# Optimization experiments

Measured on AMD Instinct MI355X. Metric: run time of the kernel, lower is better.

## Reference

```python
import jax, jax.numpy as jnp
import numpy as np

B, S, D, H, L, FF = 1, 2048, 512, 8, 4, 2048
DH = D // H


def _sincos(n, d):
    theta = 1.0 / (10000.0 ** (np.arange(0, d, 2, dtype=np.float64) / d))
    ang = np.arange(n, dtype=np.float64)[:, None] * theta[None, :]
    sin = np.repeat(np.sin(ang), 2, axis=-1).astype(np.float32)
    cos = np.repeat(np.cos(ang), 2, axis=-1).astype(np.float32)
    return jnp.asarray(sin), jnp.asarray(cos)  # [n, d]


def _rot(x):
    # rotate pairs: (x1, x2) -> (-x2, x1), interleaved
    x1, x2 = x[..., 0::2], x[..., 1::2]
    return jnp.stack([-x2, x1], axis=-1).reshape(x.shape)


def _theta_shift(x, sin, cos):
    return x * cos + _rot(x) * sin


def _decay_mask(n, h):
    # RetNet per-head decay gammas: 1 - exp(linspace(log(1/32), log(1/512), h))
    gammas = 1.0 - np.exp(np.linspace(np.log(1.0 / 32.0), np.log(1.0 / 512.0), h))
    dist = np.arange(n)[:, None] - np.arange(n)[None, :]
    m = np.where(dist >= 0, gammas[:, None, None] ** np.maximum(dist, 0), 0.0)
    return jnp.asarray(m, dtype=jnp.float32)  # [h, n, n]


def _ln(x, w, b, eps=1e-5):
    mu = x.mean(-1, keepdims=True)
    var = ((x - mu) ** 2).mean(-1, keepdims=True)
    return (x - mu) * jax.lax.rsqrt(var + eps) * w + b


def setup_inputs() -> dict:
    key = jax.random.key(0)
    ks = jax.random.split(key, 12)
    sc = 0.02
    nrm = lambda k, shp: jax.random.normal(k, shp, jnp.float32) * sc
    return {
        "x": jax.random.normal(ks[0], (B, S, D), jnp.float32),
        "pos_emb": nrm(ks[1], (5000, D)),
        "Wq": nrm(ks[2], (L, D, D)), "bq": jnp.zeros((L, D), jnp.float32),
        "Wk": nrm(ks[3], (L, D, D)), "bk": jnp.zeros((L, D), jnp.float32),
        "Wv": nrm(ks[4], (L, D, D)), "bv": jnp.zeros((L, D), jnp.float32),
        "Wg": nrm(ks[5], (L, D, D)), "bg": jnp.zeros((L, D), jnp.float32),
        "Wo": nrm(ks[6], (L, D, D)), "bo": jnp.zeros((L, D), jnp.float32),
        "ln1w": jnp.ones((L, D), jnp.float32), "ln1b": jnp.zeros((L, D), jnp.float32),
        "ln2w": jnp.ones((L, D), jnp.float32), "ln2b": jnp.zeros((L, D), jnp.float32),
        "W1": nrm(ks[7], (L, D, FF)), "b1": jnp.zeros((L, FF), jnp.float32),
        "W2": nrm(ks[8], (L, FF, D)), "b2": jnp.zeros((L, D), jnp.float32),
        "Wout": nrm(ks[9], (D, 1)), "bout": jnp.zeros((1,), jnp.float32),
    }


def reference(x, pos_emb, Wq, bq, Wk, bk, Wv, bv, Wg, bg, Wo, bo,
              ln1w, ln1b, ln2w, ln2b, W1, b1, W2, b2, Wout, bout):
    b, s, d = x.shape
    # faithful to source: pos_emb[:x.shape[0]] (requires B==1 to broadcast)
    x = x + pos_emb[: x.shape[0]]
    sin, cos = _sincos(s, DH)
    dmask = _decay_mask(s, H)  # [h, s, s]
    inv_scale = 1.0 / jnp.sqrt(jnp.float32(DH))

    def heads(t):  # [b,s,d] -> [b,h,s,dh]
        return t.reshape(b, s, H, DH).transpose(0, 2, 1, 3)

    for l in range(L):
        # --- multi-scale retention block (pre-LN) ---
        y = _ln(x, ln1w[l], ln1b[l])
        q = heads(y @ Wq[l] + bq[l])
        k = heads(y @ Wk[l] + bk[l])
        v = heads(y @ Wv[l] + bv[l])
        q = _theta_shift(q, sin, cos) * inv_scale
        k = _theta_shift(k, sin, cos)
        sim = jnp.einsum("bhnd,bhmd->bhnm", q, k) * dmask  # decay-masked QK^T
        ret = jnp.einsum("bhnm,bhmd->bhnd", sim, v)
        # per-head group norm (no affine)
        mu = ret.mean(-1, keepdims=True)
        var = ((ret - mu) ** 2).mean(-1, keepdims=True)
        ret = (ret - mu) * jax.lax.rsqrt(var + 1e-6)
        ret = ret.transpose(0, 2, 1, 3).reshape(b, s, d)
        g = jax.nn.silu(y @ Wg[l] + bg[l])
        x = x + (g * ret) @ Wo[l] + bo[l]
        # --- FFN block (pre-LN, swish) ---
        z = _ln(x, ln2w[l], ln2b[l])
        x = x + jax.nn.silu(z @ W1[l] + b1[l]) @ W2[l] + b2[l]

    return jax.nn.sigmoid(x @ Wout + bout)  # [b, s, 1]
```

## Files before the change

kernel.cpp:

```cpp
#include <hip/hip_runtime.h>
#include <math.h>
#include <stdint.h>

#define SEQ 2048
#define DMODEL 512
#define NH 8
#define DHEAD 64
#define NL 4
#define DFF 2048

typedef __attribute__((ext_vector_type(8))) short short8;
typedef __attribute__((ext_vector_type(4))) float f32x4;

__device__ __forceinline__ short f2bf(float f) {
  unsigned u = __float_as_uint(f);
  u += 0x7fffu + ((u >> 16) & 1u);
  return (short)(u >> 16);
}
__device__ __forceinline__ float silu_f(float x) { return x / (1.f + __expf(-x)); }

__device__ __forceinline__ void cp16(const void* g, void* l) {
  __builtin_amdgcn_global_load_lds(
      (const __attribute__((address_space(1))) unsigned*)(unsigned long long)(uintptr_t)g,
      (__attribute__((address_space(3))) unsigned*)(unsigned)(uintptr_t)l, 16, 0, 0);
}

struct TP { const float* src; short* dst; int rows, cols, base, lstride; };
struct TPs { TP t[7]; };
__global__ __launch_bounds__(256) void k_prep(TPs ts, float* __restrict__ sn, float* __restrict__ cs) {
  int bid = blockIdx.x;
  if (bid >= 13312) {
    int g = (bid - 13312) * 256 + threadIdx.x;
    int s = g >> 5, p = g & 31;
    double inv = pow(10000.0, -(double)p / 32.0);
    double a = (double)s * inv;
    float sv = (float)sin(a), cv = (float)cos(a);
    sn[s * DHEAD + 2 * p] = sv; sn[s * DHEAD + 2 * p + 1] = sv;
    cs[s * DHEAD + 2 * p] = cv; cs[s * DHEAD + 2 * p + 1] = cv;
    return;
  }
  int di = 6;
  while (di > 0 && bid < ts.t[di].base) --di;
  TP d = ts.t[di];
  int local = bid - d.base;
  int tx = d.cols >> 5, ty = d.rows >> 5;
  int tpz = tx * ty;
  int z = local / tpz, rem = local - z * tpz;
  int bx = (rem % tx) * 32, by = (rem / tx) * 32;
  const float* src = d.src + (size_t)z * d.rows * d.cols;
  short* dst = d.dst + (size_t)z * d.lstride;
  __shared__ float tile[32][33];
  int txi = threadIdx.x & 31, tyi = threadIdx.x >> 5;
#pragma unroll
  for (int k = 0; k < 4; ++k)
    tile[tyi + k * 8][txi] = src[(size_t)(by + tyi + k * 8) * d.cols + bx + txi];
  __syncthreads();
#pragma unroll
  for (int k = 0; k < 4; ++k)
    dst[(size_t)(bx + tyi + k * 8) * d.rows + by + txi] = f2bf(tile[txi][tyi + k * 8]);
}

__global__ __launch_bounds__(256) void k_ln(const float* __restrict__ x, const float* __restrict__ parts, int np,
                                            const float* __restrict__ w, const float* __restrict__ b,
                                            short* __restrict__ o, float eps, float* __restrict__ xout,
                                            const float* __restrict__ pos) {
  int wid = threadIdx.x >> 6, lane = threadIdx.x & 63;
  int row = blockIdx.x * 4 + wid;
  size_t base = (size_t)row * DMODEL + lane * 8;
  float4 v0 = *(const float4*)(x + base);
  float4 v1 = *(const float4*)(x + base + 4);
  if (pos) {
    float4 p0 = *(const float4*)(pos + lane * 8);
    float4 p1 = *(const float4*)(pos + lane * 8 + 4);
    v0.x += p0.x; v0.y += p0.y; v0.z += p0.z; v0.w += p0.w;
    v1.x += p1.x; v1.y += p1.y; v1.z += p1.z; v1.w += p1.w;
  }
  for (int p = 0; p < np; ++p) {
    const float* pp = parts + (size_t)p * SEQ * DMODEL;
    float4 a0 = *(const float4*)(pp + base);
    float4 a1 = *(const float4*)(pp + base + 4);
    v0.x += a0.x; v0.y += a0.y; v0.z += a0.z; v0.w += a0.w;
    v1.x += a1.x; v1.y += a1.y; v1.z += a1.z; v1.w += a1.w;
  }
  if (xout) {
    *(float4*)(xout + base) = v0;
    *(float4*)(xout + base + 4) = v1;
  }
  float sm = v0.x + v0.y + v0.z + v0.w + v1.x + v1.y + v1.z + v1.w;
  float sq = v0.x * v0.x + v0.y * v0.y + v0.z * v0.z + v0.w * v0.w +
             v1.x * v1.x + v1.y * v1.y + v1.z * v1.z + v1.w * v1.w;
#pragma unroll
  for (int m = 1; m < 64; m <<= 1) { sm += __shfl_xor(sm, m); sq += __shfl_xor(sq, m); }
  float mu = sm * (1.f / 512.f);
  float rstd = rsqrtf(sq * (1.f / 512.f) - mu * mu + eps);
  const float* wr = w + lane * 8; const float* br = b + lane * 8;
  float vals[8] = {v0.x, v0.y, v0.z, v0.w, v1.x, v1.y, v1.z, v1.w};
  short t[8] __attribute__((aligned(16)));
#pragma unroll
  for (int i = 0; i < 8; ++i) t[i] = f2bf((vals[i] - mu) * rstd * wr[i] + br[i]);
  *(int4*)(o + (size_t)row * DMODEL + lane * 8) = *(int4*)t;
}

struct GB { const short* Bt; const float* bias; void* out; int mode; };
struct GP {
  const short* A;
  const float* sn; const float* cs;
  GB b[4];
  int M, N, K, kspl, wide;
};

template <int BN>
__global__ __launch_bounds__(256) void k_gemm(GP ga) {
  constexpr int NBW = BN / 32;
  constexpr int BRND = BN / 32;
  const int z = blockIdx.z;
  const int n0 = blockIdx.x * BN, m0 = blockIdx.y * 64;
  GB gb; int k0, klen;
  if (ga.kspl > 0) { gb = ga.b[0]; k0 = z * ga.kspl; klen = ga.kspl; }
  else { gb = ga.wide ? ga.b[n0 >> 9] : ga.b[z]; k0 = 0; klen = ga.K; }
  const int K = ga.K, N = ga.N, M = ga.M;
  const int tid = threadIdx.x;
  const int w = tid >> 6, lane = tid & 63, l16 = lane & 15, quad = lane >> 4;
  const int wm = (w & 1) * 32, wn = (w >> 1) * (BN / 2);
  const int nIter = klen >> 6;

  __shared__ __align__(16) short As[2][4096];
  __shared__ __align__(16) short Bs[2][BN * 64];

  const short* Ab = ga.A + (size_t)m0 * K + k0;
  const short* Bb = gb.Bt + (size_t)n0 * K + k0;
  const int rsub = lane >> 3, cch = (lane & 7) ^ rsub;

  auto stage = [&](int buf, int it) {
#pragma unroll
    for (int c = 0; c < 2; ++c) {
      int seg = w + 4 * c;
      cp16(Ab + (size_t)(seg * 8 + rsub) * K + (it << 6) + cch * 8, &As[buf][seg * 512]);
    }
#pragma unroll
    for (int c = 0; c < BRND; ++c) {
      int seg = w + 4 * c;
      cp16(Bb + (size_t)(seg * 8 + rsub) * K + (it << 6) + cch * 8, &Bs[buf][seg * 512]);
    }
  };

  f32x4 acc[2][NBW];
#pragma unroll
  for (int a = 0; a < 2; ++a)
#pragma unroll
    for (int b = 0; b < NBW; ++b) acc[a][b] = {0.f, 0.f, 0.f, 0.f};

  stage(0, 0);
  for (int it = 0; it < nIter; ++it) {
    __syncthreads();
    if (it + 1 < nIter) stage((it + 1) & 1, it + 1);
    const short* as = As[it & 1];
    const short* bs = Bs[it & 1];
#pragma unroll
    for (int kki = 0; kki < 2; ++kki) {
      int ch = ((quad + 4 * kki) ^ (l16 & 7)) * 8;
      short8 af[2], bfv[NBW];
#pragma unroll
      for (int a = 0; a < 2; ++a) af[a] = *(const short8*)&as[(wm + a * 16 + l16) * 64 + ch];
#pragma unroll
      for (int b = 0; b < NBW; ++b) bfv[b] = *(const short8*)&bs[(wn + b * 16 + l16) * 64 + ch];
#pragma unroll
      for (int a = 0; a < 2; ++a)
#pragma unroll
        for (int b = 0; b < NBW; ++b)
          acc[a][b] = __builtin_amdgcn_mfma_f32_16x16x32_bf16(af[a], bfv[b], acc[a][b], 0, 0, 0);
    }
  }

  const int mode = gb.mode;
#pragma unroll
  for (int a = 0; a < 2; ++a) {
#pragma unroll
    for (int b = 0; b < NBW; ++b) {
      int row0 = m0 + wm + a * 16 + quad * 4;
      int col = n0 + wn + b * 16 + l16;
      int colO = ga.wide ? (col & 511) : col;
      float bi = (mode == 2 && z > 0) ? 0.f : gb.bias[colO];
      float vals[4];
#pragma unroll
      for (int r = 0; r < 4; ++r) vals[r] = acc[a][b][r] + bi;
      if (mode == 5 || mode == 6) {
        float sc = (mode == 5) ? 0.125f : 1.f;
        int d = colO & 63;
#pragma unroll
        for (int r = 0; r < 4; ++r) {
          int s = row0 + r;
          float vv = vals[r];
          float p = __shfl_xor(vv, 1);
          float rot = (colO & 1) ? p : -p;
          float o = (vv * ga.cs[s * 64 + d] + rot * ga.sn[s * 64 + d]) * sc;
          ((short*)gb.out)[(size_t)s * DMODEL + colO] = f2bf(o);
        }
      } else if (mode == 4) {
        short t4[4] __attribute__((aligned(8)));
#pragma unroll
        for (int r = 0; r < 4; ++r) t4[r] = f2bf(vals[r]);
        *(uint2*)&((short*)gb.out)[(size_t)colO * M + row0] = *(const uint2*)t4;
      } else if (mode == 0) {
#pragma unroll
        for (int r = 0; r < 4; ++r) ((float*)gb.out)[(size_t)(row0 + r) * DMODEL + colO] = vals[r];
      } else if (mode == 1) {
#pragma unroll
        for (int r = 0; r < 4; ++r) ((short*)gb.out)[(size_t)(row0 + r) * N + col] = f2bf(silu_f(vals[r]));
      } else {
        float* po = (float*)gb.out + (size_t)z * M * DMODEL;
#pragma unroll
        for (int r = 0; r < 4; ++r) po[(size_t)(row0 + r) * DMODEL + colO] = vals[r];
      }
    }
  }
}

__global__ __launch_bounds__(256) void k_attn(const short* __restrict__ qb, const short* __restrict__ kb,
                                              const short* __restrict__ vtb, float* __restrict__ r0,
                                              float* __restrict__ r1) {
  int x = blockIdx.x, hd = blockIdx.y, jc = blockIdx.z;
  int ib = jc ? (31 - x) : x;
  int t = threadIdx.x;
  int w = t >> 6, lane = t & 63, l16 = lane & 15, quad = lane >> 4;
  __shared__ __align__(16) short smem[4 * 64 * 72];
  short* qs = smem;
  short* kt = smem + 4608;
  short* vt = smem + 9216;
  short* p  = smem + 13824;

  double stepd = (log(1.0 / 512.0) - log(1.0 / 32.0)) / 7.0;
  double gam = 1.0 - exp(log(1.0 / 32.0) + hd * stepd);
  float l2g = (float)(log(gam) * 1.4426950408889634);

  for (int c = t; c < 512; c += 256) {
    int r = c >> 3, d8 = (c & 7) * 8;
    *(short8*)&qs[r * 72 + d8] = *(const short8*)&qb[(size_t)(ib * 64 + r) * DMODEL + hd * DHEAD + d8];
  }
  f32x4 oacc[4];
#pragma unroll
  for (int b = 0; b < 4; ++b) oacc[b] = {0.f, 0.f, 0.f, 0.f};

  for (int jb = jc; jb <= ib; jb += 2) {
    __syncthreads();
    for (int c = t; c < 512; c += 256) {
      int r = c >> 3, d8 = (c & 7) * 8;
      *(short8*)&kt[r * 72 + d8] = *(const short8*)&kb[(size_t)(jb * 64 + r) * DMODEL + hd * DHEAD + d8];
      *(short8*)&vt[r * 72 + d8] = *(const short8*)&vtb[(size_t)(hd * DHEAD + r) * SEQ + jb * 64 + d8];
    }
    __syncthreads();
    f32x4 sacc[4];
#pragma unroll
    for (int b = 0; b < 4; ++b) sacc[b] = {0.f, 0.f, 0.f, 0.f};
#pragma unroll
    for (int kk = 0; kk < 64; kk += 32) {
      short8 af = *(const short8*)&qs[(w * 16 + l16) * 72 + kk + quad * 8];
#pragma unroll
      for (int b = 0; b < 4; ++b) {
        short8 bf_ = *(const short8*)&kt[(b * 16 + l16) * 72 + kk + quad * 8];
        sacc[b] = __builtin_amdgcn_mfma_f32_16x16x32_bf16(af, bf_, sacc[b], 0, 0, 0);
      }
    }
    int dtile = (ib - jb) * 64;
#pragma unroll
    for (int b = 0; b < 4; ++b) {
#pragma unroll
      for (int r = 0; r < 4; ++r) {
        int iloc = w * 16 + quad * 4 + r;
        int jloc = b * 16 + l16;
        int df = dtile + iloc - jloc;
        float dec = (df < 0) ? 0.f : exp2f(l2g * (float)df);
        p[iloc * 72 + jloc] = f2bf(sacc[b][r] * dec);
      }
    }
    __syncthreads();
#pragma unroll
    for (int kk = 0; kk < 64; kk += 32) {
      short8 af = *(const short8*)&vt[(w * 16 + l16) * 72 + kk + quad * 8];
#pragma unroll
      for (int b = 0; b < 4; ++b) {
        short8 bf_ = *(const short8*)&p[(b * 16 + l16) * 72 + kk + quad * 8];
        oacc[b] = __builtin_amdgcn_mfma_f32_16x16x32_bf16(af, bf_, oacc[b], 0, 0, 0);
      }
    }
  }
  __syncthreads();
  float* obuf = (float*)smem;
#pragma unroll
  for (int b = 0; b < 4; ++b) {
#pragma unroll
    for (int r = 0; r < 4; ++r) {
      int d = w * 16 + quad * 4 + r;
      int i = b * 16 + l16;
      obuf[i * 68 + d] = oacc[b][r];
    }
  }
  __syncthreads();
  float* rp = jc ? r1 : r0;
  for (int c = t; c < 1024; c += 256) {
    int r = c >> 4, d4 = (c & 15) * 4;
    *(float4*)&rp[(size_t)(ib * 64 + r) * DMODEL + hd * DHEAD + d4] = *(const float4*)&obuf[r * 68 + d4];
  }
}

__global__ __launch_bounds__(256) void k_retgate(const float* __restrict__ r0, const float* __restrict__ r1,
                                                 const float* __restrict__ g, short* __restrict__ o) {
  int wid = threadIdx.x >> 6, lane = threadIdx.x & 63;
  int row = blockIdx.x * 4 + wid;
  int s = row >> 3, hd = row & 7;
  size_t base = (size_t)s * DMODEL + hd * DHEAD + lane;
  float v = r0[base] + r1[base];
  float sm = v, sq = v * v;
#pragma unroll
  for (int m = 1; m < 64; m <<= 1) { sm += __shfl_xor(sm, m); sq += __shfl_xor(sq, m); }
  float mu = sm * (1.f / 64.f);
  float var = sq * (1.f / 64.f) - mu * mu;
  float rn = (v - mu) * rsqrtf(var + 1e-6f);
  o[base] = f2bf(silu_f(g[base]) * rn);
}

__global__ __launch_bounds__(256) void k_final(const float* __restrict__ x, const float* __restrict__ parts, int np,
                                               const float* __restrict__ w, const float* __restrict__ bo,
                                               float* __restrict__ o) {
  int wid = threadIdx.x >> 6, lane = threadIdx.x & 63;
  int row = blockIdx.x * 4 + wid;
  size_t base = (size_t)row * DMODEL + lane * 8;
  float4 a0 = *(const float4*)(x + base), a1 = *(const float4*)(x + base + 4);
  for (int p = 0; p < np; ++p) {
    const float* pp = parts + (size_t)p * SEQ * DMODEL;
    float4 b0 = *(const float4*)(pp + base);
    float4 b1 = *(const float4*)(pp + base + 4);
    a0.x += b0.x; a0.y += b0.y; a0.z += b0.z; a0.w += b0.w;
    a1.x += b1.x; a1.y += b1.y; a1.z += b1.z; a1.w += b1.w;
  }
  float4 w0 = *(const float4*)(w + lane * 8), w1 = *(const float4*)(w + lane * 8 + 4);
  float sm = a0.x * w0.x + a0.y * w0.y + a0.z * w0.z + a0.w * w0.w +
             a1.x * w1.x + a1.y * w1.y + a1.z * w1.z + a1.w * w1.w;
#pragma unroll
  for (int m = 1; m < 64; m <<= 1) sm += __shfl_xor(sm, m);
  if (lane == 0) o[row] = 1.f / (1.f + __expf(-(sm + bo[0])));
}

extern "C" void kernel_launch(void* const* d_in, const int* in_sizes, int n_in,
                              void* d_out, int out_size, void* d_ws, size_t ws_size,
                              hipStream_t stream) {
  const float* x_in = (const float*)d_in[0];
  const float* pos = (const float*)d_in[1];
  const float* Wq = (const float*)d_in[2];  const float* bq = (const float*)d_in[3];
  const float* Wk = (const float*)d_in[4];  const float* bk = (const float*)d_in[5];
  const float* Wv = (const float*)d_in[6];  const float* bv = (const float*)d_in[7];
  const float* Wg = (const float*)d_in[8];  const float* bg = (const float*)d_in[9];
  const float* Wo = (const float*)d_in[10]; const float* bo = (const float*)d_in[11];
  const float* ln1w = (const float*)d_in[12]; const float* ln1b = (const float*)d_in[13];
  const float* ln2w = (const float*)d_in[14]; const float* ln2b = (const float*)d_in[15];
  const float* W1 = (const float*)d_in[16]; const float* b1 = (const float*)d_in[17];
  const float* W2 = (const float*)d_in[18]; const float* b2 = (const float*)d_in[19];
  const float* Wout = (const float*)d_in[20]; const float* bout = (const float*)d_in[21];
  float* out = (float*)d_out;

  char* ws = (char*)d_ws;
  size_t off = 0;
  auto alloc = [&](size_t bytes) -> void* {
    void* p = ws + off;
    off += (bytes + 255) & ~(size_t)255;
    return p;
  };
  const size_t DD = (size_t)DMODEL * DMODEL;
  const size_t SD = (size_t)SEQ * DMODEL;
  short* wqkvg = (short*)alloc((size_t)NL * 4 * DD * 2);
  short* wot = (short*)alloc((size_t)NL * DD * 2);
  short* w1t = (short*)alloc((size_t)NL * DMODEL * DFF * 2);
  short* w2t = (short*)alloc((size_t)NL * DMODEL * DFF * 2);
  float* xb = (float*)alloc(SD * 4);
  short* ybf = (short*)alloc(SD * 2);
  float* graw = (float*)alloc(SD * 4);
  short* qb = (short*)alloc(SD * 2);
  short* kb = (short*)alloc(SD * 2);
  short* vtb = (short*)alloc(SD * 2);
  float* ret0 = (float*)alloc(SD * 4);
  float* ret1 = (float*)alloc(SD * 4);
  short* grb = (short*)alloc(SD * 2);
  short* zbf = (short*)alloc(SD * 2);
  short* hbf = (short*)alloc((size_t)SEQ * DFF * 2);
  float* sint = (float*)alloc((size_t)SEQ * DHEAD * 4);
  float* cost = (float*)alloc((size_t)SEQ * DHEAD * 4);
  float* wpart = (float*)alloc(2 * SD * 4);
  float* fpart = (float*)alloc(4 * SD * 4);

  TPs tp;
  tp.t[0] = TP{Wq, wqkvg + 0 * DD, DMODEL, DMODEL, 0, (int)(4 * DD)};
  tp.t[1] = TP{Wk, wqkvg + 1 * DD, DMODEL, DMODEL, 1024, (int)(4 * DD)};
  tp.t[2] = TP{Wv, wqkvg + 2 * DD, DMODEL, DMODEL, 2048, (int)(4 * DD)};
  tp.t[3] = TP{Wg, wqkvg + 3 * DD, DMODEL, DMODEL, 3072, (int)(4 * DD)};
  tp.t[4] = TP{Wo, wot, DMODEL, DMODEL, 4096, (int)DD};
  tp.t[5] = TP{W1, w1t, DMODEL, DFF, 5120, DMODEL * DFF};
  tp.t[6] = TP{W2, w2t, DFF, DMODEL, 9216, DMODEL * DFF};
  k_prep<<<13568, 256, 0, stream>>>(tp, sint, cost);

  for (int l = 0; l < NL; ++l) {
    k_ln<<<SEQ / 4, 256, 0, stream>>>(l == 0 ? x_in : xb, fpart, l == 0 ? 0 : 4,
                                      ln1w + l * DMODEL, ln1b + l * DMODEL, ybf, 1e-5f,
                                      xb, l == 0 ? pos : nullptr);

    GP gq{};
    gq.A = ybf; gq.sn = sint; gq.cs = cost;
    gq.b[0] = GB{wqkvg + (size_t)l * 4 * DD, bq + l * DMODEL, qb, 5};
    gq.b[1] = GB{wqkvg + (size_t)l * 4 * DD, bk + l * DMODEL, kb, 6};
    gq.b[2] = GB{wqkvg + (size_t)l * 4 * DD, bv + l * DMODEL, vtb, 4};
    gq.b[3] = GB{wqkvg + (size_t)l * 4 * DD, bg + l * DMODEL, graw, 0};
    gq.M = SEQ; gq.N = 4 * DMODEL; gq.K = DMODEL; gq.kspl = 0; gq.wide = 1;
    k_gemm<128><<<dim3(16, SEQ / 64, 1), 256, 0, stream>>>(gq);

    k_attn<<<dim3(32, NH, 2), 256, 0, stream>>>(qb, kb, vtb, ret0, ret1);
    k_retgate<<<SEQ * NH / 4, 256, 0, stream>>>(ret0, ret1, graw, grb);

    GP gw{};
    gw.A = grb;
    gw.b[0] = GB{wot + l * DD, bo + l * DMODEL, wpart, 2};
    gw.M = SEQ; gw.N = DMODEL; gw.K = DMODEL; gw.kspl = 256; gw.wide = 0;
    k_gemm<64><<<dim3(DMODEL / 64, SEQ / 64, 2), 256, 0, stream>>>(gw);

    k_ln<<<SEQ / 4, 256, 0, stream>>>(xb, wpart, 2,
                                      ln2w + l * DMODEL, ln2b + l * DMODEL, zbf, 1e-5f, xb, nullptr);

    GP g1{};
    g1.A = zbf;
    g1.b[0] = GB{w1t + (size_t)l * DMODEL * DFF, b1 + l * DFF, hbf, 1};
    g1.M = SEQ; g1.N = DFF; g1.K = DMODEL; g1.kspl = 0; g1.wide = 0;
    k_gemm<128><<<dim3(DFF / 128, SEQ / 64, 1), 256, 0, stream>>>(g1);

    GP g2{};
    g2.A = hbf;
    g2.b[0] = GB{w2t + (size_t)l * DMODEL * DFF, b2 + l * DMODEL, fpart, 2};
    g2.M = SEQ; g2.N = DMODEL; g2.K = DFF; g2.kspl = 512; g2.wide = 0;
    k_gemm<64><<<dim3(DMODEL / 64, SEQ / 64, 4), 256, 0, stream>>>(g2);
  }
  k_final<<<SEQ / 4, 256, 0, stream>>>(xb, fpart, 4, Wout, bout, out);
}
```

Measured before the change: 532.3 us.

## Switch GEMM to 32x32x16 MFMA tiles and halve FFN2 split-K

Each wave in the GEMM kernel now computes its 32-row tile with 32x32x16 bf16 MFMA instructions instead of a 2xN grid of 16x16x32 ones. This cuts the number of LDS fragment loads per MFMA and the instruction count, and the epilogue is rewritten to match the new accumulator layout. Separately, the FFN down-projection split-K goes from 4 to 2 partitions, so fewer partial buffers are written and then reduced in the LN and final kernels. The cost is fewer blocks for that GEMM and therefore less parallelism.

```diff
diff --git a/kernel.cpp b/kernel.cpp
--- a/kernel.cpp
+++ b/kernel.cpp
@@ -11,6 +11,7 @@
 
 typedef __attribute__((ext_vector_type(8))) short short8;
 typedef __attribute__((ext_vector_type(4))) float f32x4;
+typedef __attribute__((ext_vector_type(16))) float f32x16;
 
 __device__ __forceinline__ short f2bf(float f) {
   unsigned u = __float_as_uint(f);
@@ -111,7 +112,7 @@
 
 template <int BN>
 __global__ __launch_bounds__(256) void k_gemm(GP ga) {
-  constexpr int NBW = BN / 32;
+  constexpr int NB = BN / 64;
   constexpr int BRND = BN / 32;
   const int z = blockIdx.z;
   const int n0 = blockIdx.x * BN, m0 = blockIdx.y * 64;
@@ -120,7 +121,8 @@
   else { gb = ga.wide ? ga.b[n0 >> 9] : ga.b[z]; k0 = 0; klen = ga.K; }
   const int K = ga.K, N = ga.N, M = ga.M;
   const int tid = threadIdx.x;
-  const int w = tid >> 6, lane = tid & 63, l16 = lane & 15, quad = lane >> 4;
+  const int w = tid >> 6, lane = tid & 63;
+  const int l32 = lane & 31, half = lane >> 5;
   const int wm = (w & 1) * 32, wn = (w >> 1) * (BN / 2);
   const int nIter = klen >> 6;
 
@@ -144,11 +146,7 @@
     }
   };
 
-  f32x4 acc[2][NBW];
-#pragma unroll
-  for (int a = 0; a < 2; ++a)
-#pragma unroll
-    for (int b = 0; b < NBW; ++b) acc[a][b] = {0.f, 0.f, 0.f, 0.f};
+  f32x16 acc[NB] = {};
 
   stage(0, 0);
   for (int it = 0; it < nIter; ++it) {
@@ -157,60 +155,62 @@
     const short* as = As[it & 1];
     const short* bs = Bs[it & 1];
 #pragma unroll
-    for (int kki = 0; kki < 2; ++kki) {
-      int ch = ((quad + 4 * kki) ^ (l16 & 7)) * 8;
-      short8 af[2], bfv[NBW];
-#pragma unroll
-      for (int a = 0; a < 2; ++a) af[a] = *(const short8*)&as[(wm + a * 16 + l16) * 64 + ch];
-#pragma unroll
-      for (int b = 0; b < NBW; ++b) bfv[b] = *(const short8*)&bs[(wn + b * 16 + l16) * 64 + ch];
-#pragma unroll
-      for (int a = 0; a < 2; ++a)
-#pragma unroll
-        for (int b = 0; b < NBW; ++b)
-          acc[a][b] = __builtin_amdgcn_mfma_f32_16x16x32_bf16(af[a], bfv[b], acc[a][b], 0, 0, 0);
+    for (int s = 0; s < 4; ++s) {
+      int slot = ((2 * s + half) ^ (l32 & 7)) * 8;
+      short8 af = *(const short8*)&as[(wm + l32) * 64 + slot];
+#pragma unroll
+      for (int b = 0; b < NB; ++b) {
+        short8 bf_ = *(const short8*)&bs[(wn + b * 32 + l32) * 64 + slot];
+        acc[b] = __builtin_amdgcn_mfma_f32_32x32x16_bf16(af, bf_, acc[b], 0, 0, 0);
+      }
     }
   }
 
   const int mode = gb.mode;
 #pragma unroll
-  for (int a = 0; a < 2; ++a) {
-#pragma unroll
-    for (int b = 0; b < NBW; ++b) {
-      int row0 = m0 + wm + a * 16 + quad * 4;
-      int col = n0 + wn + b * 16 + l16;
-      int colO = ga.wide ? (col & 511) : col;
-      float bi = (mode == 2 && z > 0) ? 0.f : gb.bias[colO];
-      float vals[4];
-#pragma unroll
-      for (int r = 0; r < 4; ++r) vals[r] = acc[a][b][r] + bi;
-      if (mode == 5 || mode == 6) {
-        float sc = (mode == 5) ? 0.125f : 1.f;
-        int d = colO & 63;
-#pragma unroll
-        for (int r = 0; r < 4; ++r) {
-          int s = row0 + r;
-          float vv = vals[r];
-          float p = __shfl_xor(vv, 1);
-          float rot = (colO & 1) ? p : -p;
-          float o = (vv * ga.cs[s * 64 + d] + rot * ga.sn[s * 64 + d]) * sc;
-          ((short*)gb.out)[(size_t)s * DMODEL + colO] = f2bf(o);
-        }
-      } else if (mode == 4) {
+  for (int b = 0; b < NB; ++b) {
+    int col = n0 + wn + b * 32 + l32;
+    int colO = ga.wide ? (col & 511) : col;
+    float bi = (mode == 2 && z > 0) ? 0.f : gb.bias[colO];
+    if (mode == 5 || mode == 6) {
+      float sc = (mode == 5) ? 0.125f : 1.f;
+      int d = colO & 63;
+#pragma unroll
+      for (int r = 0; r < 16; ++r) {
+        int row = m0 + wm + (r & 3) + 8 * (r >> 2) + 4 * half;
+        float vv = acc[b][r] + bi;
+        float p = __shfl_xor(vv, 1);
+        float rot = (colO & 1) ? p : -p;
+        float o = (vv * ga.cs[row * 64 + d] + rot * ga.sn[row * 64 + d]) * sc;
+        ((short*)gb.out)[(size_t)row * DMODEL + colO] = f2bf(o);
+      }
+    } else if (mode == 4) {
+#pragma unroll
+      for (int g = 0; g < 4; ++g) {
         short t4[4] __attribute__((aligned(8)));
 #pragma unroll
-        for (int r = 0; r < 4; ++r) t4[r] = f2bf(vals[r]);
+        for (int j = 0; j < 4; ++j) t4[j] = f2bf(acc[b][g * 4 + j] + bi);
+        int row0 = m0 + wm + 8 * g + 4 * half;
         *(uint2*)&((short*)gb.out)[(size_t)colO * M + row0] = *(const uint2*)t4;
-      } else if (mode == 0) {
-#pragma unroll
-        for (int r = 0; r < 4; ++r) ((float*)gb.out)[(size_t)(row0 + r) * DMODEL + colO] = vals[r];
-      } else if (mode == 1) {
-#pragma unroll
-        for (int r = 0; r < 4; ++r) ((short*)gb.out)[(size_t)(row0 + r) * N + col] = f2bf(silu_f(vals[r]));
-      } else {
-        float* po = (float*)gb.out + (size_t)z * M * DMODEL;
-#pragma unroll
-        for (int r = 0; r < 4; ++r) po[(size_t)(row0 + r) * DMODEL + colO] = vals[r];
+      }
+    } else if (mode == 0) {
+#pragma unroll
+      for (int r = 0; r < 16; ++r) {
+        int row = m0 + wm + (r & 3) + 8 * (r >> 2) + 4 * half;
+        ((float*)gb.out)[(size_t)row * DMODEL + colO] = acc[b][r] + bi;
+      }
+    } else if (mode == 1) {
+#pragma unroll
+      for (int r = 0; r < 16; ++r) {
+        int row = m0 + wm + (r & 3) + 8 * (r >> 2) + 4 * half;
+        ((short*)gb.out)[(size_t)row * N + col] = f2bf(silu_f(acc[b][r] + bi));
+      }
+    } else {
+      float* po = (float*)gb.out + (size_t)z * M * DMODEL;
+#pragma unroll
+      for (int r = 0; r < 16; ++r) {
+        int row = m0 + wm + (r & 3) + 8 * (r >> 2) + 4 * half;
+        po[(size_t)row * DMODEL + colO] = acc[b][r] + bi;
       }
     }
   }
@@ -385,7 +385,7 @@
   float* sint = (float*)alloc((size_t)SEQ * DHEAD * 4);
   float* cost = (float*)alloc((size_t)SEQ * DHEAD * 4);
   float* wpart = (float*)alloc(2 * SD * 4);
-  float* fpart = (float*)alloc(4 * SD * 4);
+  float* fpart = (float*)alloc(2 * SD * 4);
 
   TPs tp;
   tp.t[0] = TP{Wq, wqkvg + 0 * DD, DMODEL, DMODEL, 0, (int)(4 * DD)};
@@ -398,7 +398,7 @@
   k_prep<<<13568, 256, 0, stream>>>(tp, sint, cost);
 
   for (int l = 0; l < NL; ++l) {
-    k_ln<<<SEQ / 4, 256, 0, stream>>>(l == 0 ? x_in : xb, fpart, l == 0 ? 0 : 4,
+    k_ln<<<SEQ / 4, 256, 0, stream>>>(l == 0 ? x_in : xb, fpart, l == 0 ? 0 : 2,
                                       ln1w + l * DMODEL, ln1b + l * DMODEL, ybf, 1e-5f,
                                       xb, l == 0 ? pos : nullptr);
 
@@ -432,8 +432,8 @@
     GP g2{};
     g2.A = hbf;
     g2.b[0] = GB{w2t + (size_t)l * DMODEL * DFF, b2 + l * DMODEL, fpart, 2};
-    g2.M = SEQ; g2.N = DMODEL; g2.K = DFF; g2.kspl = 512; g2.wide = 0;
-    k_gemm<64><<<dim3(DMODEL / 64, SEQ / 64, 4), 256, 0, stream>>>(g2);
-  }
-  k_final<<<SEQ / 4, 256, 0, stream>>>(xb, fpart, 4, Wout, bout, out);
-}
+    g2.M = SEQ; g2.N = DMODEL; g2.K = DFF; g2.kspl = 1024; g2.wide = 0;
+    k_gemm<64><<<dim3(DMODEL / 64, SEQ / 64, 2), 256, 0, stream>>>(g2);
+  }
+  k_final<<<SEQ / 4, 256, 0, stream>>>(xb, fpart, 2, Wout, bout, out);
+}
```

After: 500.2 us. -6.0%, faster.
